# Optimization experiments

Hardware: AMD Instinct MI355X
Metric: run time of the kernel (lower is better)

The kernel has to match this reference:

```python
import jax, jax.numpy as jnp
import numpy as np

N_HEAD = 16

def setup_inputs() -> dict:
    key = jax.random.key(0)
    ks = jax.random.split(key, 9)
    B, T, C = 1, 4096, 1024
    s = 1.0 / np.sqrt(C)
    x = jax.random.normal(ks[0], (B, T, C), dtype=jnp.float32)
    Wq = jax.random.uniform(ks[1], (C, C), jnp.float32, -s, s)
    bq = jax.random.uniform(ks[2], (C,), jnp.float32, -s, s)
    Wk = jax.random.uniform(ks[3], (C, C), jnp.float32, -s, s)
    bk = jax.random.uniform(ks[4], (C,), jnp.float32, -s, s)
    Wv = jax.random.uniform(ks[5], (C, C), jnp.float32, -s, s)
    bv = jax.random.uniform(ks[6], (C,), jnp.float32, -s, s)
    Wp = jax.random.uniform(ks[7], (C, C), jnp.float32, -s, s)
    bp = jax.random.uniform(ks[8], (C,), jnp.float32, -s, s)
    return {"x": x, "Wq": Wq, "bq": bq, "Wk": Wk, "bk": bk,
            "Wv": Wv, "bv": bv, "Wp": Wp, "bp": bp}

def reference(x, Wq, bq, Wk, bk, Wv, bv, Wp, bp):
    B, T, C = x.shape
    H = N_HEAD
    D = C // H
    # projections -> (B, H, T, D)
    def proj(W, b):
        return (x @ W.T + b).reshape(B, T, H, D).transpose(0, 2, 1, 3)
    q, k, v = proj(Wq, bq), proj(Wk, bk), proj(Wv, bv)
    scale = 1.0 / np.sqrt(D).astype(np.float32)
    att = jnp.einsum('bhtd,bhsd->bhts', q, k) * scale  # (B,H,T,T)
    causal = jnp.tril(jnp.ones((T, T), dtype=bool))
    att = jnp.where(causal[None, None], att, -jnp.inf)
    att = jax.nn.softmax(att, axis=-1)
    y = jnp.einsum('bhts,bhsd->bhtd', att, v)  # (B,H,T,D)
    y = y.transpose(0, 2, 1, 3).reshape(B, T, C)
    return y @ Wp.T + bp
```

## Files before the change

### kernel.cpp

```cpp
#include <hip/hip_runtime.h>
#include <hip/hip_bf16.h>
#include <math.h>

typedef __bf16 bf16x8 __attribute__((ext_vector_type(8)));
typedef __bf16 bf16x4 __attribute__((ext_vector_type(4)));
typedef float f32x4 __attribute__((ext_vector_type(4)));

#define MFMA_BF16 __builtin_amdgcn_mfma_f32_16x16x32_bf16

#define QSCALE 0.18033688011112042f

__device__ inline void async_load16(const __hip_bfloat16* g, __hip_bfloat16* l) {
    __builtin_amdgcn_global_load_lds(
        (const __attribute__((address_space(1))) unsigned int*)g,
        (__attribute__((address_space(3))) unsigned int*)l,
        16, 0, 0);
}

__device__ inline int sig(int x) {
    return (x & ~12) | ((x & 4) << 1) | ((x & 8) >> 1);
}

__device__ inline unsigned int pack_bf16_trunc(float lo, float hi) {
    return __builtin_amdgcn_perm(__float_as_uint(hi), __float_as_uint(lo),
                                 0x07060302u);
}

__global__ __launch_bounds__(256) void convert_all(
    const float* __restrict__ x,
    const float* __restrict__ Wq, const float* __restrict__ Wk,
    const float* __restrict__ Wv, const float* __restrict__ Wp,
    __hip_bfloat16* __restrict__ xb,
    __hip_bfloat16* __restrict__ Wqb, __hip_bfloat16* __restrict__ Wkb,
    __hip_bfloat16* __restrict__ Wvb, __hip_bfloat16* __restrict__ Wpb,
    int nx, int nw)
{
    const int xblocks = nx >> 11;
    const int wblocks = nw >> 11;
    int b = blockIdx.x;
    const float* in;
    __hip_bfloat16* out;
    int i;
    if (b < xblocks) {
        in = x; out = xb; i = (b * 256 + threadIdx.x) * 8;
    } else {
        b -= xblocks;
        const int w = b / wblocks, bb = b - w * wblocks;
        in  = w == 0 ? Wq : w == 1 ? Wk : w == 2 ? Wv : Wp;
        out = w == 0 ? Wqb : w == 1 ? Wkb : w == 2 ? Wvb : Wpb;
        i = (bb * 256 + threadIdx.x) * 8;
    }
    const float4 a = *(const float4*)(in + i);
    const float4 c = *(const float4*)(in + i + 4);
    __hip_bfloat16 tmp[8];
    tmp[0] = __float2bfloat16(a.x); tmp[1] = __float2bfloat16(a.y);
    tmp[2] = __float2bfloat16(a.z); tmp[3] = __float2bfloat16(a.w);
    tmp[4] = __float2bfloat16(c.x); tmp[5] = __float2bfloat16(c.y);
    tmp[6] = __float2bfloat16(c.z); tmp[7] = __float2bfloat16(c.w);
    *(bf16x8*)(out + i) = *(const bf16x8*)tmp;
}

__global__ __launch_bounds__(256) void gemm_qkv(
    const __hip_bfloat16* __restrict__ A,
    const __hip_bfloat16* __restrict__ B,
    const float* __restrict__ bq, const float* __restrict__ bk, const float* __restrict__ bv,
    __hip_bfloat16* __restrict__ Qo, __hip_bfloat16* __restrict__ Ko,
    __hip_bfloat16* __restrict__ Vt,
    int M, int K)
{
    __shared__ __align__(16) __hip_bfloat16 smem[2 * 128 * 64];
    __hip_bfloat16* As = smem;
    __hip_bfloat16* Bs = smem + 128 * 64;

    const int tid  = threadIdx.x;
    const int lane = tid & 63;
    const int wave = tid >> 6;
    const int l15  = lane & 15;
    const int quad = lane >> 4;
    const int m0 = blockIdx.x * 128;
    const int n0 = blockIdx.y * 128;
    const int wr = wave >> 1, wc = wave & 1;
    const int sel = n0 >> 10;

    f32x4 acc[4][4] = {};

    int srow[4], scol[4];
    #pragma unroll
    for (int i = 0; i < 4; ++i) {
        const int c = tid + 256 * i;
        srow[i] = c >> 3;
        scol[i] = ((c & 7) ^ (srow[i] & 7)) * 8;
    }

    for (int k0 = 0; k0 < K; k0 += 64) {
        __syncthreads();
        #pragma unroll
        for (int i = 0; i < 4; ++i) {
            async_load16(A + (size_t)(m0 + srow[i]) * K + k0 + scol[i],
                         As + (size_t)(tid + 256 * i) * 8);
            async_load16(B + (size_t)(n0 + srow[i]) * K + k0 + scol[i],
                         Bs + (size_t)(tid + 256 * i) * 8);
        }
        __syncthreads();

        #pragma unroll
        for (int kd = 0; kd < 2; ++kd) {
            bf16x8 af[4], bfr[4];
            #pragma unroll
            for (int mi = 0; mi < 4; ++mi) {
                const int row = wr * 64 + mi * 16 + l15;
                af[mi] = *(const bf16x8*)(
                    As + row * 64 + (((kd * 4 + quad) ^ (row & 7)) << 3));
            }
            #pragma unroll
            for (int ni = 0; ni < 4; ++ni) {
                const int row = wc * 64 + ni * 16 + l15;
                bfr[ni] = *(const bf16x8*)(
                    Bs + row * 64 + (((kd * 4 + quad) ^ (row & 7)) << 3));
            }
            #pragma unroll
            for (int mi = 0; mi < 4; ++mi)
                #pragma unroll
                for (int ni = 0; ni < 4; ++ni)
                    acc[mi][ni] = MFMA_BF16(af[mi], bfr[ni], acc[mi][ni], 0, 0, 0);
        }
    }

    if (sel == 2) {
        __syncthreads();
        #pragma unroll
        for (int ni = 0; ni < 4; ++ni) {
            const int lc = wc * 64 + ni * 16 + l15;
            const float bias = bv[(n0 + lc) & 1023];
            #pragma unroll
            for (int mi = 0; mi < 4; ++mi) {
                const int mb = wr * 64 + mi * 16 + quad * 4;
                const int g = mb >> 3, off = mb & 7;
                __hip_bfloat16 t[4];
                #pragma unroll
                for (int r = 0; r < 4; ++r)
                    t[r] = __float2bfloat16(acc[mi][ni][r] + bias);
                *(bf16x4*)(smem + lc * 128 + ((g ^ (lc & 15)) << 3) + off)
                    = *(const bf16x4*)t;
            }
        }
        __syncthreads();
        const int cc0 = n0 & 1023;
        #pragma unroll
        for (int i = 0; i < 8; ++i) {
            const int q = tid + 256 * i;
            const int ch = q >> 4, mg = q & 15;
            bf16x8 v = *(const bf16x8*)(smem + ch * 128 + ((mg ^ (ch & 15)) << 3));
            *(bf16x8*)(Vt + (size_t)(cc0 + ch) * M + m0 + mg * 8) = v;
        }
    } else {
        __hip_bfloat16* dst = sel == 0 ? Qo : Ko;
        const float* bptr   = sel == 0 ? bq : bk;
        const float sc      = sel == 0 ? QSCALE : 1.0f;
        #pragma unroll
        for (int ni = 0; ni < 4; ++ni) {
            const int cc = (n0 + wc * 64 + ni * 16 + l15) & 1023;
            const float bias = bptr[cc];
            #pragma unroll
            for (int mi = 0; mi < 4; ++mi) {
                const int row = m0 + wr * 64 + mi * 16 + quad * 4;
                #pragma unroll
                for (int r = 0; r < 4; ++r)
                    dst[(size_t)(row + r) * 1024 + cc] =
                        __float2bfloat16((acc[mi][ni][r] + bias) * sc);
            }
        }
    }
}

__global__ __launch_bounds__(256) void gemm_out_f32(
    const __hip_bfloat16* __restrict__ A,
    const __hip_bfloat16* __restrict__ B,
    const float* __restrict__ bias,
    float* __restrict__ Cf,
    int M, int N, int K)
{
    __shared__ __align__(16) __hip_bfloat16 As[64 * 64];
    __shared__ __align__(16) __hip_bfloat16 Bs[128 * 64];

    const int tid  = threadIdx.x;
    const int lane = tid & 63;
    const int wave = tid >> 6;
    const int l15  = lane & 15;
    const int quad = lane >> 4;
    const int m0 = blockIdx.x * 64;
    const int n0 = blockIdx.y * 128;
    const int wr = wave >> 1, wc = wave & 1;

    f32x4 acc[2][4] = {};

    int srow[4], scol[4];
    #pragma unroll
    for (int i = 0; i < 4; ++i) {
        const int c = tid + 256 * i;
        srow[i] = c >> 3;
        scol[i] = ((c & 7) ^ (srow[i] & 7)) * 8;
    }

    for (int k0 = 0; k0 < K; k0 += 64) {
        __syncthreads();
        #pragma unroll
        for (int i = 0; i < 2; ++i)
            async_load16(A + (size_t)(m0 + srow[i]) * K + k0 + scol[i],
                         As + (size_t)(tid + 256 * i) * 8);
        #pragma unroll
        for (int i = 0; i < 4; ++i)
            async_load16(B + (size_t)(n0 + srow[i]) * K + k0 + scol[i],
                         Bs + (size_t)(tid + 256 * i) * 8);
        __syncthreads();

        #pragma unroll
        for (int kd = 0; kd < 2; ++kd) {
            bf16x8 af[2], bfr[4];
            #pragma unroll
            for (int mi = 0; mi < 2; ++mi) {
                const int row = wr * 32 + mi * 16 + l15;
                af[mi] = *(const bf16x8*)(
                    As + row * 64 + (((kd * 4 + quad) ^ (row & 7)) << 3));
            }
            #pragma unroll
            for (int ni = 0; ni < 4; ++ni) {
                const int row = wc * 64 + ni * 16 + l15;
                bfr[ni] = *(const bf16x8*)(
                    Bs + row * 64 + (((kd * 4 + quad) ^ (row & 7)) << 3));
            }
            #pragma unroll
            for (int mi = 0; mi < 2; ++mi)
                #pragma unroll
                for (int ni = 0; ni < 4; ++ni)
                    acc[mi][ni] = MFMA_BF16(af[mi], bfr[ni], acc[mi][ni], 0, 0, 0);
        }
    }

    #pragma unroll
    for (int ni = 0; ni < 4; ++ni) {
        const int col = n0 + wc * 64 + ni * 16 + l15;
        const float bv = bias[col];
        #pragma unroll
        for (int mi = 0; mi < 2; ++mi) {
            const int row = m0 + wr * 32 + mi * 16 + quad * 4;
            #pragma unroll
            for (int r = 0; r < 4; ++r)
                Cf[(size_t)(row + r) * N + col] = acc[mi][ni][r] + bv;
        }
    }
}

__global__ __launch_bounds__(512, 4) void attn_causal(
    const __hip_bfloat16* __restrict__ Q,
    const __hip_bfloat16* __restrict__ K,
    const __hip_bfloat16* __restrict__ Vt,
    __hip_bfloat16* __restrict__ PoB,
    float* __restrict__ PlB,
    int T, int C)
{
    const int h  = blockIdx.y;
    const int bx = blockIdx.x;
    const int j  = bx & 7;
    const int sq = bx >> 3;
    const int tid  = threadIdx.x;
    const int w    = tid >> 6;
    const int lane = tid & 63;
    const int l15  = lane & 15;
    const int quad = lane >> 4;

    const size_t TCs = (size_t)T * C;
    const size_t HT  = (size_t)T * 16;
    __hip_bfloat16* Po = PoB + (size_t)sq * TCs;
    float* Pl = PlB + (size_t)sq * HT;

    const int len1 = j + 1, len2 = 16 - j;
    const int tile1 = j,    tile2 = 15 - j;
    const int kb1 = len1 * sq, kb2 = len2 * sq;

    __shared__ __align__(16) __hip_bfloat16 Ks[2][64 * 64];
    __shared__ __align__(16) __hip_bfloat16 Vts[2][64 * 64];

    const int r0 = tid >> 3, g0 = ((tid & 7) ^ (r0 & 7)) * 8;
    const __hip_bfloat16* Kg0 = K + (size_t)sig(r0) * C + h * 64 + g0;
    const __hip_bfloat16* Vg0 = Vt + (size_t)(h * 64 + r0) * T + g0;

    int koff[2][4], voff[2][4];
    #pragma unroll
    for (int kd = 0; kd < 2; ++kd)
        #pragma unroll
        for (int sb = 0; sb < 4; ++sb) {
            const int kappa = 32 * (sb & 1) + 8 * (l15 >> 2) + 4 * (sb >> 1) + (l15 & 3);
            const int rho = sig(kappa);
            koff[kd][sb] = rho * 64 + (((kd * 4 + quad) ^ (rho & 7)) << 3);
        }
    #pragma unroll
    for (int kk = 0; kk < 2; ++kk)
        #pragma unroll
        for (int db = 0; db < 4; ++db) {
            const int vrow = db * 16 + l15;
            voff[kk][db] = vrow * 64 + (((kk * 4 + quad) ^ (vrow & 7)) << 3);
        }

    bf16x8 ones;
    #pragma unroll
    for (int jj = 0; jj < 8; ++jj) ones[jj] = (__bf16)1.0f;

    int qbase = tile1 * 256 + w * 32;
    bf16x8 aq[2][2];
    #pragma unroll
    for (int rb = 0; rb < 2; ++rb)
        #pragma unroll
        for (int kd = 0; kd < 2; ++kd)
            aq[rb][kd] = *(const bf16x8*)(
                Q + (size_t)(qbase + rb * 16 + l15) * C + h * 64 + kd * 32 + quad * 8);

    f32x4 o[2][4] = {};
    f32x4 lacc[2] = {};

    {
        const size_t so = (size_t)kb1 << 6;
        async_load16(Kg0 + so * C, &Ks[0][tid * 8]);
        async_load16(Vg0 + so, &Vts[0][tid * 8]);
    }

    for (int it = 0; it < 17; ++it) {
        const int kb = (it < len1) ? (kb1 + it) : (kb2 + it - len1);
        const int s0 = kb << 6;
        __syncthreads();
        const int cur = it & 1;
        if (it + 1 < 17) {
            const int kbn = (it + 1 < len1) ? (kb1 + it + 1) : (kb2 + it + 1 - len1);
            const size_t so = (size_t)kbn << 6;
            async_load16(Kg0 + so * C, &Ks[cur ^ 1][tid * 8]);
            async_load16(Vg0 + so, &Vts[cur ^ 1][tid * 8]);
        }

        if (it == len1) {
            #pragma unroll
            for (int rb = 0; rb < 2; ++rb) {
                const int row = qbase + rb * 16 + l15;
                #pragma unroll
                for (int db = 0; db < 4; ++db) {
                    __hip_bfloat16 t[4];
                    #pragma unroll
                    for (int r = 0; r < 4; ++r)
                        t[r] = __float2bfloat16(o[rb][db][r]);
                    *(bf16x4*)(Po + (size_t)row * C + h * 64 + db * 16 + quad * 4)
                        = *(const bf16x4*)t;
                    o[rb][db] = (f32x4){0.f, 0.f, 0.f, 0.f};
                }
                if (quad == 0)
                    Pl[(size_t)h * T + row] = lacc[rb][0];
                lacc[rb] = (f32x4){0.f, 0.f, 0.f, 0.f};
            }
            qbase = tile2 * 256 + w * 32;
            #pragma unroll
            for (int rb = 0; rb < 2; ++rb)
                #pragma unroll
                for (int kd = 0; kd < 2; ++kd)
                    aq[rb][kd] = *(const bf16x8*)(
                        Q + (size_t)(qbase + rb * 16 + l15) * C + h * 64 + kd * 32 + quad * 8);
        }

        if (s0 <= qbase + 31) {
            f32x4 sv[2][4] = {};
            #pragma unroll
            for (int kd = 0; kd < 2; ++kd)
                #pragma unroll
                for (int sb = 0; sb < 4; ++sb) {
                    bf16x8 ak = *(const bf16x8*)(&Ks[cur][koff[kd][sb]]);
                    sv[0][sb] = MFMA_BF16(ak, aq[0][kd], sv[0][sb], 0, 0, 0);
                    sv[1][sb] = MFMA_BF16(ak, aq[1][kd], sv[1][sb], 0, 0, 0);
                }

            const bool diag = (s0 + 63 > qbase);
            bf16x8 bp[2][2];
            #pragma unroll
            for (int rb = 0; rb < 2; ++rb) {
                float pv[4][4];
                #pragma unroll
                for (int sb = 0; sb < 4; ++sb)
                    #pragma unroll
                    for (int r = 0; r < 4; ++r)
                        pv[sb][r] = __builtin_amdgcn_exp2f(sv[rb][sb][r]);
                if (diag) {
                    const int thr = qbase + rb * 16 + l15 - s0 - 8 * quad;
                    #pragma unroll
                    for (int sb = 0; sb < 4; ++sb)
                        #pragma unroll
                        for (int r = 0; r < 4; ++r) {
                            const int c = 32 * (sb & 1) + 4 * (sb >> 1) + r;
                            pv[sb][r] = (c <= thr) ? pv[sb][r] : 0.f;
                        }
                }
                #pragma unroll
                for (int kk = 0; kk < 2; ++kk) {
                    union { unsigned int u[4]; bf16x8 v; } pk;
                    pk.u[0] = pack_bf16_trunc(pv[kk][0], pv[kk][1]);
                    pk.u[1] = pack_bf16_trunc(pv[kk][2], pv[kk][3]);
                    pk.u[2] = pack_bf16_trunc(pv[kk + 2][0], pv[kk + 2][1]);
                    pk.u[3] = pack_bf16_trunc(pv[kk + 2][2], pv[kk + 2][3]);
                    bp[rb][kk] = pk.v;
                }
            }

            lacc[0] = MFMA_BF16(ones, bp[0][0], lacc[0], 0, 0, 0);
            lacc[0] = MFMA_BF16(ones, bp[0][1], lacc[0], 0, 0, 0);
            lacc[1] = MFMA_BF16(ones, bp[1][0], lacc[1], 0, 0, 0);
            lacc[1] = MFMA_BF16(ones, bp[1][1], lacc[1], 0, 0, 0);

            #pragma unroll
            for (int kk = 0; kk < 2; ++kk)
                #pragma unroll
                for (int db = 0; db < 4; ++db) {
                    bf16x8 av = *(const bf16x8*)(&Vts[cur][voff[kk][db]]);
                    o[0][db] = MFMA_BF16(av, bp[0][kk], o[0][db], 0, 0, 0);
                    o[1][db] = MFMA_BF16(av, bp[1][kk], o[1][db], 0, 0, 0);
                }
        }
    }

    #pragma unroll
    for (int rb = 0; rb < 2; ++rb) {
        const int row = qbase + rb * 16 + l15;
        #pragma unroll
        for (int db = 0; db < 4; ++db) {
            __hip_bfloat16 t[4];
            #pragma unroll
            for (int r = 0; r < 4; ++r)
                t[r] = __float2bfloat16(o[rb][db][r]);
            *(bf16x4*)(Po + (size_t)row * C + h * 64 + db * 16 + quad * 4)
                = *(const bf16x4*)t;
        }
        if (quad == 0)
            Pl[(size_t)h * T + row] = lacc[rb][0];
    }
}

__global__ __launch_bounds__(256) void merge_y(
    const __hip_bfloat16* __restrict__ PoB, const float* __restrict__ PlB,
    __hip_bfloat16* __restrict__ Y, int T, int C)
{
    const size_t i = ((size_t)blockIdx.x * 256 + threadIdx.x) * 8;
    const int row = (int)(i / C);
    const int h   = ((int)(i % C)) >> 6;
    const size_t TC = (size_t)T * C;
    const size_t HT = (size_t)T * 16;
    float acc[8] = {};
    float l = 0.f;
    #pragma unroll
    for (int z = 0; z < 4; ++z) {
        bf16x8 a = *(const bf16x8*)(PoB + z * TC + i);
        #pragma unroll
        for (int r = 0; r < 8; ++r)
            acc[r] += (float)(((const __bf16*)&a)[r]);
        l += PlB[z * HT + (size_t)h * T + row];
    }
    const float inv = 1.0f / l;
    __hip_bfloat16 t[8];
    #pragma unroll
    for (int r = 0; r < 8; ++r)
        t[r] = __float2bfloat16(acc[r] * inv);
    *(bf16x8*)(Y + i) = *(const bf16x8*)t;
}

extern "C" void kernel_launch(void* const* d_in, const int* in_sizes, int n_in,
                              void* d_out, int out_size, void* d_ws, size_t ws_size,
                              hipStream_t stream)
{
    const float* x  = (const float*)d_in[0];
    const float* Wq = (const float*)d_in[1];
    const float* bq = (const float*)d_in[2];
    const float* Wk = (const float*)d_in[3];
    const float* bk = (const float*)d_in[4];
    const float* Wv = (const float*)d_in[5];
    const float* bv = (const float*)d_in[6];
    const float* Wp = (const float*)d_in[7];
    const float* bp = (const float*)d_in[8];

    const int C = 1024;
    const int T = in_sizes[0] / C;
    const int H = 16;
    const size_t TC = (size_t)T * C;
    const size_t CC = (size_t)C * C;

    __hip_bfloat16* xb  = (__hip_bfloat16*)d_ws;
    __hip_bfloat16* Wqb = xb + TC;
    __hip_bfloat16* Wkb = Wqb + CC;
    __hip_bfloat16* Wvb = Wkb + CC;
    __hip_bfloat16* Wpb = Wvb + CC;
    __hip_bfloat16* Qw  = Wpb + CC;
    __hip_bfloat16* Kw  = Qw + TC;
    __hip_bfloat16* Vtw = Kw + TC;
    __hip_bfloat16* PoB = Vtw + TC;
    float* PlB = (float*)(PoB + 4 * TC);
    __hip_bfloat16* Yw  = xb;
    float* out = (float*)d_out;

    convert_all<<<(int)(TC / 2048 + 4 * CC / 2048), 256, 0, stream>>>(
        x, Wq, Wk, Wv, Wp, xb, Wqb, Wkb, Wvb, Wpb, (int)TC, (int)CC);

    gemm_qkv<<<dim3(T / 128, 3072 / 128), 256, 0, stream>>>(
        xb, Wqb, bq, bk, bv, Qw, Kw, Vtw, T, C);

    attn_causal<<<dim3(32, H), 512, 0, stream>>>(
        Qw, Kw, Vtw, PoB, PlB, T, C);

    merge_y<<<(int)(TC / 8 / 256), 256, 0, stream>>>(
        PoB, PlB, Yw, T, C);

    gemm_out_f32<<<dim3(T / 64, C / 128), 256, 0, stream>>>(
        Yw, Wpb, bp, out, T, C, C);
}
```

Baseline: 201.6 us.

## Software-pipeline attention loop: overlap QK of tile i with PV of tile i-1

Restructures the attention inner loop so that each iteration issues the QK^T MFMAs for the current key block together with the PV and row-sum MFMAs for the previous block, with the exp/mask/pack step moved after them. K/V shared-memory buffering grows from double to quadruple, with prefetch two blocks ahead, and MFMA sections are wrapped in s_setprio. The goal is to hide exp latency and global-load latency behind matrix work. In exchange it doubles LDS use, which may lower occupancy, and adds an epilogue for the last block.

```diff
diff --git a/kernel.cpp b/kernel.cpp
--- a/kernel.cpp
+++ b/kernel.cpp
@@ -278,8 +278,8 @@
     const int tile1 = j,    tile2 = 15 - j;
     const int kb1 = len1 * sq, kb2 = len2 * sq;
 
-    __shared__ __align__(16) __hip_bfloat16 Ks[2][64 * 64];
-    __shared__ __align__(16) __hip_bfloat16 Vts[2][64 * 64];
+    __shared__ __align__(16) __hip_bfloat16 Ks[4][64 * 64];
+    __shared__ __align__(16) __hip_bfloat16 Vts[4][64 * 64];
 
     const int r0 = tid >> 3, g0 = ((tid & 7) ^ (r0 & 7)) * 8;
     const __hip_bfloat16* Kg0 = K + (size_t)sig(r0) * C + h * 64 + g0;
@@ -306,6 +306,14 @@
     #pragma unroll
     for (int jj = 0; jj < 8; ++jj) ones[jj] = (__bf16)1.0f;
 
+    auto stage = [&](int idx) {
+        const int kb = (idx < len1) ? (kb1 + idx) : (kb2 + idx - len1);
+        const size_t so = (size_t)kb << 6;
+        const int sl = idx & 3;
+        async_load16(Kg0 + so * C, &Ks[sl][tid * 8]);
+        async_load16(Vg0 + so, &Vts[sl][tid * 8]);
+    };
+
     int qbase = tile1 * 256 + w * 32;
     bf16x8 aq[2][2];
     #pragma unroll
@@ -317,26 +325,69 @@
 
     f32x4 o[2][4] = {};
     f32x4 lacc[2] = {};
-
-    {
-        const size_t so = (size_t)kb1 << 6;
-        async_load16(Kg0 + so * C, &Ks[0][tid * 8]);
-        async_load16(Vg0 + so, &Vts[0][tid * 8]);
-    }
-
-    for (int it = 0; it < 17; ++it) {
-        const int kb = (it < len1) ? (kb1 + it) : (kb2 + it - len1);
-        const int s0 = kb << 6;
-        __syncthreads();
-        const int cur = it & 1;
-        if (it + 1 < 17) {
-            const int kbn = (it + 1 < len1) ? (kb1 + it + 1) : (kb2 + it + 1 - len1);
-            const size_t so = (size_t)kbn << 6;
-            async_load16(Kg0 + so * C, &Ks[cur ^ 1][tid * 8]);
-            async_load16(Vg0 + so, &Vts[cur ^ 1][tid * 8]);
-        }
-
-        if (it == len1) {
+    bf16x8 bp[2][2];
+    bool livePrev = false;
+
+    stage(0);
+    stage(1);
+
+    for (int i = 0; i < 17; ++i) {
+        __syncthreads();
+        if (i + 2 < 17) stage(i + 2);
+
+        const int ti  = (i < len1) ? tile1 : tile2;
+        const int qbQ = ti * 256 + w * 32;
+        const int kb  = (i < len1) ? (kb1 + i) : (kb2 + i - len1);
+        const int s0  = kb << 6;
+        const bool live = (s0 <= qbQ + 31);
+
+        if (i == len1) {
+            #pragma unroll
+            for (int rb = 0; rb < 2; ++rb)
+                #pragma unroll
+                for (int kd = 0; kd < 2; ++kd)
+                    aq[rb][kd] = *(const bf16x8*)(
+                        Q + (size_t)(qbQ + rb * 16 + l15) * C + h * 64 + kd * 32 + quad * 8);
+        }
+
+        __builtin_amdgcn_s_setprio(1);
+
+        f32x4 sv[2][4];
+        if (live) {
+            #pragma unroll
+            for (int rb = 0; rb < 2; ++rb)
+                #pragma unroll
+                for (int sb = 0; sb < 4; ++sb)
+                    sv[rb][sb] = (f32x4){0.f, 0.f, 0.f, 0.f};
+            #pragma unroll
+            for (int kd = 0; kd < 2; ++kd)
+                #pragma unroll
+                for (int sb = 0; sb < 4; ++sb) {
+                    bf16x8 ak = *(const bf16x8*)(&Ks[i & 3][koff[kd][sb]]);
+                    sv[0][sb] = MFMA_BF16(ak, aq[0][kd], sv[0][sb], 0, 0, 0);
+                    sv[1][sb] = MFMA_BF16(ak, aq[1][kd], sv[1][sb], 0, 0, 0);
+                }
+        }
+
+        if (livePrev) {
+            const int sp = (i - 1) & 3;
+            lacc[0] = MFMA_BF16(ones, bp[0][0], lacc[0], 0, 0, 0);
+            lacc[0] = MFMA_BF16(ones, bp[0][1], lacc[0], 0, 0, 0);
+            lacc[1] = MFMA_BF16(ones, bp[1][0], lacc[1], 0, 0, 0);
+            lacc[1] = MFMA_BF16(ones, bp[1][1], lacc[1], 0, 0, 0);
+            #pragma unroll
+            for (int kk = 0; kk < 2; ++kk)
+                #pragma unroll
+                for (int db = 0; db < 4; ++db) {
+                    bf16x8 av = *(const bf16x8*)(&Vts[sp][voff[kk][db]]);
+                    o[0][db] = MFMA_BF16(av, bp[0][kk], o[0][db], 0, 0, 0);
+                    o[1][db] = MFMA_BF16(av, bp[1][kk], o[1][db], 0, 0, 0);
+                }
+        }
+
+        __builtin_amdgcn_s_setprio(0);
+
+        if (i == len1) {
             #pragma unroll
             for (int rb = 0; rb < 2; ++rb) {
                 const int row = qbase + rb * 16 + l15;
@@ -355,27 +406,10 @@
                 lacc[rb] = (f32x4){0.f, 0.f, 0.f, 0.f};
             }
             qbase = tile2 * 256 + w * 32;
-            #pragma unroll
-            for (int rb = 0; rb < 2; ++rb)
-                #pragma unroll
-                for (int kd = 0; kd < 2; ++kd)
-                    aq[rb][kd] = *(const bf16x8*)(
-                        Q + (size_t)(qbase + rb * 16 + l15) * C + h * 64 + kd * 32 + quad * 8);
-        }
-
-        if (s0 <= qbase + 31) {
-            f32x4 sv[2][4] = {};
-            #pragma unroll
-            for (int kd = 0; kd < 2; ++kd)
-                #pragma unroll
-                for (int sb = 0; sb < 4; ++sb) {
-                    bf16x8 ak = *(const bf16x8*)(&Ks[cur][koff[kd][sb]]);
-                    sv[0][sb] = MFMA_BF16(ak, aq[0][kd], sv[0][sb], 0, 0, 0);
-                    sv[1][sb] = MFMA_BF16(ak, aq[1][kd], sv[1][sb], 0, 0, 0);
-                }
-
-            const bool diag = (s0 + 63 > qbase);
-            bf16x8 bp[2][2];
+        }
+
+        if (live) {
+            const bool diag = (s0 + 63 > qbQ);
             #pragma unroll
             for (int rb = 0; rb < 2; ++rb) {
                 float pv[4][4];
@@ -385,7 +419,7 @@
                     for (int r = 0; r < 4; ++r)
                         pv[sb][r] = __builtin_amdgcn_exp2f(sv[rb][sb][r]);
                 if (diag) {
-                    const int thr = qbase + rb * 16 + l15 - s0 - 8 * quad;
+                    const int thr = qbQ + rb * 16 + l15 - s0 - 8 * quad;
                     #pragma unroll
                     for (int sb = 0; sb < 4; ++sb)
                         #pragma unroll
@@ -404,21 +438,24 @@
                     bp[rb][kk] = pk.v;
                 }
             }
-
-            lacc[0] = MFMA_BF16(ones, bp[0][0], lacc[0], 0, 0, 0);
-            lacc[0] = MFMA_BF16(ones, bp[0][1], lacc[0], 0, 0, 0);
-            lacc[1] = MFMA_BF16(ones, bp[1][0], lacc[1], 0, 0, 0);
-            lacc[1] = MFMA_BF16(ones, bp[1][1], lacc[1], 0, 0, 0);
-
-            #pragma unroll
-            for (int kk = 0; kk < 2; ++kk)
-                #pragma unroll
-                for (int db = 0; db < 4; ++db) {
-                    bf16x8 av = *(const bf16x8*)(&Vts[cur][voff[kk][db]]);
-                    o[0][db] = MFMA_BF16(av, bp[0][kk], o[0][db], 0, 0, 0);
-                    o[1][db] = MFMA_BF16(av, bp[1][kk], o[1][db], 0, 0, 0);
-                }
-        }
+        }
+        livePrev = live;
+    }
+
+    if (livePrev) {
+        const int sp = 16 & 3;
+        lacc[0] = MFMA_BF16(ones, bp[0][0], lacc[0], 0, 0, 0);
+        lacc[0] = MFMA_BF16(ones, bp[0][1], lacc[0], 0, 0, 0);
+        lacc[1] = MFMA_BF16(ones, bp[1][0], lacc[1], 0, 0, 0);
+        lacc[1] = MFMA_BF16(ones, bp[1][1], lacc[1], 0, 0, 0);
+        #pragma unroll
+        for (int kk = 0; kk < 2; ++kk)
+            #pragma unroll
+            for (int db = 0; db < 4; ++db) {
+                bf16x8 av = *(const bf16x8*)(&Vts[sp][voff[kk][db]]);
+                o[0][db] = MFMA_BF16(av, bp[0][kk], o[0][db], 0, 0, 0);
+                o[1][db] = MFMA_BF16(av, bp[1][kk], o[1][db], 0, 0, 0);
+            }
     }
 
     #pragma unroll
```

After: 230.0 us. +14.1%, slower.

## Deepen attention K/V prefetch to four LDS stages and remap workgroups across XCDs

Applied to the files above, without the earlier changes.

Replaces the double-buffered K/V tile loads in the causal attention kernel with a 4-slot ring that keeps two tiles in flight, using explicit vmcnt waits plus s_barrier instead of __syncthreads. This aims to hide more global-load latency behind the MFMA work. It also remaps the linear workgroup id so that consecutive work items land on the same XCD chunk, which should improve L2 reuse of K/V for a head. LDS use doubles, which may cut occupancy, and the hand-counted vmcnt values must match the number of loads in flight.

```diff
diff --git a/kernel.cpp b/kernel.cpp
--- a/kernel.cpp
+++ b/kernel.cpp
@@ -259,8 +259,12 @@
     float* __restrict__ PlB,
     int T, int C)
 {
-    const int h  = blockIdx.y;
-    const int bx = blockIdx.x;
+    const int nwg  = (int)(gridDim.x * gridDim.y);
+    const int chunk = nwg >> 3;
+    const int lin  = (int)(blockIdx.x + gridDim.x * blockIdx.y);
+    const int work = (lin & 7) * chunk + (lin >> 3);
+    const int h  = work >> 5;
+    const int bx = work & 31;
     const int j  = bx & 7;
     const int sq = bx >> 3;
     const int tid  = threadIdx.x;
@@ -278,8 +282,8 @@
     const int tile1 = j,    tile2 = 15 - j;
     const int kb1 = len1 * sq, kb2 = len2 * sq;
 
-    __shared__ __align__(16) __hip_bfloat16 Ks[2][64 * 64];
-    __shared__ __align__(16) __hip_bfloat16 Vts[2][64 * 64];
+    __shared__ __align__(16) __hip_bfloat16 Ks[4][64 * 64];
+    __shared__ __align__(16) __hip_bfloat16 Vts[4][64 * 64];
 
     const int r0 = tid >> 3, g0 = ((tid & 7) ^ (r0 & 7)) * 8;
     const __hip_bfloat16* Kg0 = K + (size_t)sig(r0) * C + h * 64 + g0;
@@ -318,23 +322,29 @@
     f32x4 o[2][4] = {};
     f32x4 lacc[2] = {};
 
-    {
-        const size_t so = (size_t)kb1 << 6;
-        async_load16(Kg0 + so * C, &Ks[0][tid * 8]);
-        async_load16(Vg0 + so, &Vts[0][tid * 8]);
-    }
+    auto stage = [&](int idx) {
+        const int kb = (idx < len1) ? (kb1 + idx) : (kb2 + idx - len1);
+        const size_t so = (size_t)kb << 6;
+        const int sl = idx & 3;
+        async_load16(Kg0 + so * C, &Ks[sl][tid * 8]);
+        async_load16(Vg0 + so, &Vts[sl][tid * 8]);
+    };
+
+    stage(0);
+    stage(1);
 
     for (int it = 0; it < 17; ++it) {
+        if (it + 2 < 17) stage(it + 2);
+        if (it < 15)
+            asm volatile("s_waitcnt vmcnt(4)\n\ts_barrier" ::: "memory");
+        else if (it == 15)
+            asm volatile("s_waitcnt vmcnt(2)\n\ts_barrier" ::: "memory");
+        else
+            asm volatile("s_waitcnt vmcnt(0)\n\ts_barrier" ::: "memory");
+
+        const int cur = it & 3;
         const int kb = (it < len1) ? (kb1 + it) : (kb2 + it - len1);
         const int s0 = kb << 6;
-        __syncthreads();
-        const int cur = it & 1;
-        if (it + 1 < 17) {
-            const int kbn = (it + 1 < len1) ? (kb1 + it + 1) : (kb2 + it + 1 - len1);
-            const size_t so = (size_t)kbn << 6;
-            async_load16(Kg0 + so * C, &Ks[cur ^ 1][tid * 8]);
-            async_load16(Vg0 + so, &Vts[cur ^ 1][tid * 8]);
-        }
 
         if (it == len1) {
             #pragma unroll
```

Measured after the change: 199.4 us. Within noise of the previous version (-1.1%).
